# Optimization experiments

Measured on AMD Instinct MI355X. Metric: run time of the kernel, lower is better.

The kernel has to match this reference:

```python
import jax, jax.numpy as jnp
import numpy as np

B = 65536
CEP_ORDER = 99          # M
IR_LENGTH = 512         # N


def setup_inputs() -> dict:
    key = jax.random.key(0)
    # scale cepstral coeffs like real cepstra (decaying with quefrency) for stability
    scale = 0.5 / (1.0 + jnp.arange(CEP_ORDER + 1, dtype=jnp.float32))
    c = jax.random.normal(key, (B, CEP_ORDER + 1), dtype=jnp.float32) * scale
    return {"c": c}


def reference(c):
    # Oppenheim recursion: h[0] = exp(c[0]); h[n] = (1/n) sum_{m=1}^{min(n,M)} m*c[m]*h[n-m]
    Bc, M1 = c.shape
    M = M1 - 1
    N = IR_LENGTH
    arange = jnp.arange(1, M + 1, dtype=c.dtype)
    c1f = (c[:, 1:] * arange)[:, ::-1]        # flipped weighted cepstrum, [B, M]
    h0 = jnp.exp(c[:, 0])                      # [B]
    # buffer holds h[n-M : n]; zeros for negative indices
    buf0 = jnp.concatenate([jnp.zeros((Bc, M - 1), c.dtype), h0[:, None]], axis=1)

    def step(buf, n):
        hn = jnp.einsum('bm,bm->b', buf, c1f) / n      # [B]
        buf = jnp.concatenate([buf[:, 1:], hn[:, None]], axis=1)
        return buf, hn

    ns = jnp.arange(1, N, dtype=c.dtype)
    _, hs = jax.lax.scan(step, buf0, ns)               # hs: [N-1, B]
    h = jnp.concatenate([h0[:, None], hs.T], axis=1)   # [B, N]
    return h
```

## Files before the change

### kernel.cpp

```cpp
#include <hip/hip_runtime.h>
#include <math.h>


#define NROWS   128
#define STRIDE  129

__device__ __forceinline__ float dpp_xor1(float x) {
    int r = __builtin_amdgcn_mov_dpp(__float_as_int(x), 0xB1, 0xF, 0xF, false);
    return __int_as_float(r);
}

__global__ __launch_bounds__(256, 2)
void cep2ir_kernel(const float* __restrict__ c, float* __restrict__ out) {
    __shared__ float stage[NROWS * STRIDE];
    const int t = threadIdx.x;
    const int lrow = t >> 1;
    const bool isA = (t & 1) == 0;
    const int rowbase = blockIdx.x * NROWS;
    const float* cb = c + (size_t)(rowbase + lrow) * 100;
    float* outb = out + (size_t)rowbase * 512;

    float e[52];
    {
        const float4* c4 = reinterpret_cast<const float4*>(cb);
        const int f4b = isA ? 0 : 12;
#pragma unroll
        for (int i = 0; i < 13; ++i) {
            const float4 v = c4[f4b + i];
            e[4 * i + 0] = v.x; e[4 * i + 1] = v.y;
            e[4 * i + 2] = v.z; e[4 * i + 3] = v.w;
        }
    }
    float w[50];
#pragma unroll
    for (int k = 0; k < 49; ++k)
        w[k] = (isA ? e[k + 1] : e[k + 3]) * (isA ? (float)(k + 1) : (float)(k + 51));
    w[49] = isA ? e[50] * 50.0f : 0.0f;

    const float h0 = expf(e[0]);

    float hh[66];
#pragma unroll
    for (int k = 0; k < 66; ++k) hh[k] = 0.0f;
    hh[16] = isA ? h0 : 0.0f;

    if (isA) stage[lrow * STRIDE] = h0;

    float fn = 1.0f;
    float carry = 0.0f;

#pragma unroll 1
    for (int p = 0; p < 4; ++p) {
        float* sp = &stage[lrow * STRIDE + 1];
#pragma unroll 1
        for (int gg = 0; gg < 8; ++gg) {
            float rn[16];
#pragma unroll
            for (int j = 0; j < 16; ++j) rn[j] = __builtin_amdgcn_rcpf(fn + (float)j);

            float hnLast = 0.0f;
#pragma unroll
            for (int j = 0; j < 16; ++j) {
                float a0 = 0.f, a1 = 0.f;
#pragma unroll
                for (int k = 0; k < 50; ++k) {
                    const float prod = w[k] * hh[k + 16 - j];
                    if ((k & 1) == 0) a0 += prod; else a1 += prod;
                }
                const float asum = a0 + a1;
                const float hn = (asum + dpp_xor1(asum)) * rn[j];
                if (isA) sp[j] = hn;
                hh[15 - j] = isA ? hn : hh[15 - j];
                if (j == 15) hnLast = hn;
            }
            carry = hnLast;

            float bv[16];
#pragma unroll
            for (int jj = 0; jj < 16; ++jj) bv[jj] = dpp_xor1(hh[34 + jj]);
#pragma unroll
            for (int k = 65; k >= 16; --k) hh[k] = hh[k - 16];
#pragma unroll
            for (int jj = 0; jj < 16; ++jj) hh[jj] = bv[jj];
            fn += 16.0f;
            sp += 16;
        }
        __syncthreads();
#pragma unroll 1
        for (int i = 0; i < 64; ++i) {
            const int idx = i * 256 + t;
            const int r = idx >> 7;
            const int cc = idx & 127;
            outb[(size_t)r * 512 + p * 128 + cc] = stage[r * STRIDE + cc];
        }
        __syncthreads();
        if (p < 3 && isA) stage[lrow * STRIDE] = carry;
    }
}

extern "C" void kernel_launch(void* const* d_in, const int* in_sizes, int n_in,
                              void* d_out, int out_size, void* d_ws, size_t ws_size,
                              hipStream_t stream) {
    const float* c = (const float*)d_in[0];
    float* out = (float*)d_out;
    cep2ir_kernel<<<512, 256, 0, stream>>>(c, out);
}
```

Measured before the change: 111.6 us.

## Split each row's recursion across four lanes instead of two

```diff
diff --git a/kernel.cpp b/kernel.cpp
--- a/kernel.cpp
+++ b/kernel.cpp
@@ -2,49 +2,63 @@
 #include <math.h>
 
 
-#define NROWS   128
+#define NROWS   64
 #define STRIDE  129
 
 __device__ __forceinline__ float dpp_xor1(float x) {
-    int r = __builtin_amdgcn_mov_dpp(__float_as_int(x), 0xB1, 0xF, 0xF, false);
-    return __int_as_float(r);
+    return __int_as_float(__builtin_amdgcn_mov_dpp(__float_as_int(x), 0xB1, 0xF, 0xF, false));
+}
+__device__ __forceinline__ float dpp_xor2(float x) {
+    return __int_as_float(__builtin_amdgcn_mov_dpp(__float_as_int(x), 0x4E, 0xF, 0xF, false));
+}
+__device__ __forceinline__ float dpp_shr1(float x) {
+    return __int_as_float(__builtin_amdgcn_mov_dpp(__float_as_int(x), 0x111, 0xF, 0xF, false));
 }
 
-__global__ __launch_bounds__(256, 2)
+__global__ __launch_bounds__(256, 4)
 void cep2ir_kernel(const float* __restrict__ c, float* __restrict__ out) {
     __shared__ float stage[NROWS * STRIDE];
     const int t = threadIdx.x;
-    const int lrow = t >> 1;
-    const bool isA = (t & 1) == 0;
+    const int l = t & 3;
+    const int lrow = t >> 2;
+    const bool isBase = (l == 0);
     const int rowbase = blockIdx.x * NROWS;
     const float* cb = c + (size_t)(rowbase + lrow) * 100;
     float* outb = out + (size_t)rowbase * 512;
 
-    float e[52];
+    float e[28];
     {
         const float4* c4 = reinterpret_cast<const float4*>(cb);
-        const int f4b = isA ? 0 : 12;
+        const int b0 = 6 * l + (l == 3 ? 1 : 0);
 #pragma unroll
-        for (int i = 0; i < 13; ++i) {
-            const float4 v = c4[f4b + i];
+        for (int i = 0; i < 7; ++i) {
+            int blk = b0 + i;
+            if (l == 3 && i == 6) blk = 24;
+            const float4 v = c4[blk];
             e[4 * i + 0] = v.x; e[4 * i + 1] = v.y;
             e[4 * i + 2] = v.z; e[4 * i + 3] = v.w;
         }
     }
-    float w[50];
+    float w[25];
+    {
+        const float lf = (float)l;
 #pragma unroll
-    for (int k = 0; k < 49; ++k)
-        w[k] = (isA ? e[k + 1] : e[k + 3]) * (isA ? (float)(k + 1) : (float)(k + 51));
-    w[49] = isA ? e[50] * 50.0f : 0.0f;
+        for (int k = 0; k < 25; ++k) {
+            const float ce = (l == 0) ? e[k + 1] : (l == 1) ? e[k + 2]
+                           : (l == 2) ? e[k + 3] : e[k];
+            w[k] = ce * (25.0f * lf + (float)(k + 1));
+        }
+        if (l == 3) w[24] = 0.0f;
+    }
 
     const float h0 = expf(e[0]);
 
-    float hh[66];
+    float hh[41];
 #pragma unroll
-    for (int k = 0; k < 66; ++k) hh[k] = 0.0f;
-    hh[16] = isA ? h0 : 0.0f;
+    for (int k = 0; k < 41; ++k) hh[k] = 0.0f;
+    hh[16] = isBase ? h0 : 0.0f;
 
-    if (isA) stage[lrow * STRIDE] = h0;
+    if (isBase) stage[lrow * STRIDE] = h0;
 
     float fn = 1.0f;
     float carry = 0.0f;
@@ -58,28 +72,30 @@
 #pragma unroll
             for (int j = 0; j < 16; ++j) rn[j] = __builtin_amdgcn_rcpf(fn + (float)j);
 
-            float hnLast = 0.0f;
 #pragma unroll
             for (int j = 0; j < 16; ++j) {
                 float a0 = 0.f, a1 = 0.f;
 #pragma unroll
-                for (int k = 0; k < 50; ++k) {
-                    const float prod = w[k] * hh[k + 16 - j];
-                    if ((k & 1) == 0) a0 += prod; else a1 += prod;
+                for (int k = 0; k < 25; ++k) {
+                    if ((k & 1) == 0) a0 = __builtin_fmaf(w[k], hh[k + 16 - j], a0);
+                    else              a1 = __builtin_fmaf(w[k], hh[k + 16 - j], a1);
                 }
-                const float asum = a0 + a1;
-                const float hn = (asum + dpp_xor1(asum)) * rn[j];
-                if (isA) sp[j] = hn;
-                hh[15 - j] = isA ? hn : hh[15 - j];
-                if (j == 15) hnLast = hn;
+                float s = a0 + a1;
+                s += dpp_xor1(s);
+                s += dpp_xor2(s);
+                const float hn = s * rn[j];
+                hh[15 - j] = isBase ? hn : hh[15 - j];
+                if (j == 15) carry = hn;
             }
-            carry = hnLast;
-
+            if (isBase) {
+#pragma unroll
+                for (int j = 0; j < 16; ++j) sp[j] = hh[15 - j];
+            }
             float bv[16];
 #pragma unroll
-            for (int jj = 0; jj < 16; ++jj) bv[jj] = dpp_xor1(hh[34 + jj]);
+            for (int jj = 0; jj < 16; ++jj) bv[jj] = dpp_shr1(hh[9 + jj]);
 #pragma unroll
-            for (int k = 65; k >= 16; --k) hh[k] = hh[k - 16];
+            for (int k = 40; k >= 16; --k) hh[k] = hh[k - 16];
 #pragma unroll
             for (int jj = 0; jj < 16; ++jj) hh[jj] = bv[jj];
             fn += 16.0f;
@@ -87,14 +103,14 @@
         }
         __syncthreads();
 #pragma unroll 1
-        for (int i = 0; i < 64; ++i) {
+        for (int i = 0; i < 32; ++i) {
             const int idx = i * 256 + t;
             const int r = idx >> 7;
             const int cc = idx & 127;
             outb[(size_t)r * 512 + p * 128 + cc] = stage[r * STRIDE + cc];
         }
         __syncthreads();
-        if (p < 3 && isA) stage[lrow * STRIDE] = carry;
+        if (p < 3 && isBase) stage[lrow * STRIDE] = carry;
     }
 }
 
@@ -103,5 +119,5 @@
                               hipStream_t stream) {
     const float* c = (const float*)d_in[0];
     float* out = (float*)d_out;
-    cep2ir_kernel<<<512, 256, 0, stream>>>(c, out);
+    cep2ir_kernel<<<1024, 256, 0, stream>>>(c, out);
 }
```

Result: slower. 123.2 us (+10.4%).

## Widen register recurrence window to 32 steps and precompute reciprocals in LDS

Applied to the files above, without the earlier changes.

```diff
diff --git a/kernel.cpp b/kernel.cpp
--- a/kernel.cpp
+++ b/kernel.cpp
@@ -6,19 +6,25 @@
 #define STRIDE  129
 
 __device__ __forceinline__ float dpp_xor1(float x) {
-    int r = __builtin_amdgcn_mov_dpp(__float_as_int(x), 0xB1, 0xF, 0xF, false);
-    return __int_as_float(r);
+    return __int_as_float(__builtin_amdgcn_mov_dpp(__float_as_int(x), 0xB1, 0xF, 0xF, false));
 }
 
 __global__ __launch_bounds__(256, 2)
 void cep2ir_kernel(const float* __restrict__ c, float* __restrict__ out) {
     __shared__ float stage[NROWS * STRIDE];
+    __shared__ float4 rn4[128];
     const int t = threadIdx.x;
     const int lrow = t >> 1;
     const bool isA = (t & 1) == 0;
     const int rowbase = blockIdx.x * NROWS;
     const float* cb = c + (size_t)(rowbase + lrow) * 100;
     float* outb = out + (size_t)rowbase * 512;
+
+    {
+        float* rt = reinterpret_cast<float*>(rn4);
+        rt[t]       = __builtin_amdgcn_rcpf((float)(t + 1));
+        rt[t + 256] = __builtin_amdgcn_rcpf((float)(t + 257));
+    }
 
     float e[52];
     {
@@ -39,51 +45,51 @@
 
     const float h0 = expf(e[0]);
 
-    float hh[66];
+    float hh[82];
 #pragma unroll
-    for (int k = 0; k < 66; ++k) hh[k] = 0.0f;
-    hh[16] = isA ? h0 : 0.0f;
+    for (int k = 0; k < 82; ++k) hh[k] = 0.0f;
+    hh[32] = isA ? h0 : 0.0f;
 
     if (isA) stage[lrow * STRIDE] = h0;
-
-    float fn = 1.0f;
-    float carry = 0.0f;
+    __syncthreads();
 
 #pragma unroll 1
     for (int p = 0; p < 4; ++p) {
-        float* sp = &stage[lrow * STRIDE + 1];
 #pragma unroll 1
-        for (int gg = 0; gg < 8; ++gg) {
-            float rn[16];
+        for (int gg = 0; gg < 4; ++gg) {
+            float4 r4[8];
+            {
+                const float4* rp = &rn4[8 * (4 * p + gg)];
 #pragma unroll
-            for (int j = 0; j < 16; ++j) rn[j] = __builtin_amdgcn_rcpf(fn + (float)j);
-
-            float hnLast = 0.0f;
+                for (int i = 0; i < 8; ++i) r4[i] = rp[i];
+            }
 #pragma unroll
-            for (int j = 0; j < 16; ++j) {
+            for (int j = 0; j < 32; ++j) {
                 float a0 = 0.f, a1 = 0.f;
 #pragma unroll
                 for (int k = 0; k < 50; ++k) {
-                    const float prod = w[k] * hh[k + 16 - j];
-                    if ((k & 1) == 0) a0 += prod; else a1 += prod;
+                    if ((k & 1) == 0) a0 = __builtin_fmaf(w[k], hh[k + 32 - j], a0);
+                    else              a1 = __builtin_fmaf(w[k], hh[k + 32 - j], a1);
                 }
-                const float asum = a0 + a1;
-                const float hn = (asum + dpp_xor1(asum)) * rn[j];
-                if (isA) sp[j] = hn;
-                hh[15 - j] = isA ? hn : hh[15 - j];
-                if (j == 15) hnLast = hn;
+                float s = a0 + a1;
+                s += dpp_xor1(s);
+                const float rn = (j & 2) ? ((j & 1) ? r4[j >> 2].w : r4[j >> 2].z)
+                                         : ((j & 1) ? r4[j >> 2].y : r4[j >> 2].x);
+                const float hn = s * rn;
+                hh[31 - j] = isA ? hn : hh[31 - j];
             }
-            carry = hnLast;
-
-            float bv[16];
+            if (isA) {
+                float* sc = &stage[lrow * STRIDE + 1 + 32 * gg];
 #pragma unroll
-            for (int jj = 0; jj < 16; ++jj) bv[jj] = dpp_xor1(hh[34 + jj]);
+                for (int j = 0; j < 32; ++j) sc[j] = hh[31 - j];
+            }
+            float bv[32];
 #pragma unroll
-            for (int k = 65; k >= 16; --k) hh[k] = hh[k - 16];
+            for (int i = 0; i < 32; ++i) bv[i] = dpp_xor1(hh[18 + i]);
 #pragma unroll
-            for (int jj = 0; jj < 16; ++jj) hh[jj] = bv[jj];
-            fn += 16.0f;
-            sp += 16;
+            for (int k = 81; k >= 32; --k) hh[k] = hh[k - 32];
+#pragma unroll
+            for (int i = 0; i < 32; ++i) hh[i] = bv[i];
         }
         __syncthreads();
 #pragma unroll 1
@@ -94,7 +100,7 @@
             outb[(size_t)r * 512 + p * 128 + cc] = stage[r * STRIDE + cc];
         }
         __syncthreads();
-        if (p < 3 && isA) stage[lrow * STRIDE] = carry;
+        if (p < 3 && isA) stage[lrow * STRIDE] = hh[32];
     }
 }
 
```

After: 104.3 us. -6.5%, faster.
